# Optimization experiments

Measured on AMD Instinct MI355X. Metric: run time of the kernel, lower is better.

Reference implementation:

```python
import jax, jax.numpy as jnp
import numpy as np

NUM_USERS = 4096
NUM_ITEMS = 4096
NUM_CLASSES = 5
INPUT_DIM = 64
H0 = 64   # hidden[0]
H1 = 32   # hidden[1]
BU = 2048
BV = 2048


def setup_inputs() -> dict:
    key = jax.random.key(0)
    ks = jax.random.split(key, 9)
    ridx = jax.random.randint(ks[0], (NUM_USERS, NUM_ITEMS), 0, NUM_CLASSES * 10)
    ratings = (jnp.arange(NUM_CLASSES)[:, None, None] == ridx[None]).astype(jnp.float32)
    u = jax.random.randint(ks[1], (BU,), 0, NUM_USERS)
    v = jax.random.randint(ks[2], (BV,), 0, NUM_ITEMS)
    u_emb = jax.random.normal(ks[3], (NUM_USERS, INPUT_DIM), jnp.float32) * 0.1
    v_emb = jax.random.normal(ks[4], (NUM_ITEMS, INPUT_DIM), jnp.float32) * 0.1
    gc_w = jax.random.normal(ks[5], (NUM_CLASSES, INPUT_DIM, H0), jnp.float32) / np.sqrt(INPUT_DIM)
    gc_b = jnp.zeros((NUM_CLASSES, H0), jnp.float32)
    dense_w = jax.random.normal(ks[6], (H0, H1), jnp.float32) / np.sqrt(H0)
    dense_b = jnp.zeros((H1,), jnp.float32)
    dec_w = jax.random.normal(ks[7], (NUM_CLASSES, H1, H1), jnp.float32) / np.sqrt(H1)
    return dict(u=u, v=v, ratings=ratings, u_emb=u_emb, v_emb=v_emb,
                gc_w=gc_w, gc_b=gc_b, dense_w=dense_w, dense_b=dense_b, dec_w=dec_w)


def reference(u, v, ratings, u_emb, v_emb, gc_w, gc_b, dense_w, dense_b, dec_w):
    bu = u.shape[0]
    # m = index_select(index_select(ratings, 1, u), 2, v)  -> [C, bu, bv]
    m = ratings[:, u][:, :, v]
    ue = u_emb[u]                      # [bu, D]
    ve = v_emb[v]                      # [bv, D]
    # Degree normalization exactly as in the torch code:
    # du = |sum over dim1 then dim0| -> per-item counts [bv]; di -> per-user counts [bu]
    du = jnp.abs(jnp.sum(m, axis=(0, 1)))
    di = jnp.abs(jnp.sum(m, axis=(0, 2)))
    c = jnp.concatenate([du, di])      # [bv + bu] (requires bu == bv, as in original)
    c = jnp.where(c > 0, 1.0 / c, 0.0)
    x = jnp.concatenate([ue, ve], axis=0)              # [bu+bv, D]
    # Per-class graph convolution, summed over rating classes.
    support = jnp.einsum('nd,cdh->cnh', x, gc_w)       # [C, N, H0]
    su, sv = support[:, :bu], support[:, bu:]
    agg_u = jnp.einsum('cuv,cvh->cuh', m, sv)          # users aggregate items
    agg_v = jnp.einsum('cuv,cuh->cvh', m, su)          # items aggregate users
    agg = jnp.concatenate([agg_u, agg_v], axis=1)      # [C, N, H0]
    z = jnp.sum(c[None, :, None] * agg + gc_b[:, None, :], axis=0)
    z = jax.nn.relu(z)
    hidden = jax.nn.sigmoid(z @ dense_w + dense_b)     # [N, H1]
    hu, hv = hidden[:bu], hidden[bu:]
    # Bilinear decoder: per-class logits u^T W_c v  -> [C, bu, bv]
    logits = jnp.einsum('ud,cde,ve->cuv', hu, dec_w, hv)
    probs = jax.nn.softmax(logits, axis=0)
    classes = jnp.arange(NUM_CLASSES, dtype=hidden.dtype)
    m_hat = jnp.einsum('c,cuv->uv', classes, probs)    # expected rating
    observed = jnp.sum(m, axis=0)                      # [bu, bv] in {0,1}
    n_obs = jnp.maximum(jnp.sum(observed), 1.0)
    logp = jax.nn.log_softmax(logits, axis=0)
    loss = -jnp.sum(m * logp) / n_obs
    pred = jnp.argmax(logits, axis=0)
    true = jnp.argmax(m, axis=0)
    accuracy = jnp.sum((pred == true) * observed) / n_obs
    return m_hat, loss, accuracy
```

## Files before the change

kernel.cpp:

```cpp
#include <hip/hip_runtime.h>
#include <hip/hip_bf16.h>
#include <cstdint>

#define RST 16777216
typedef unsigned short u16;
typedef unsigned char u8;
typedef __attribute__((ext_vector_type(8))) short short8v;
typedef __attribute__((ext_vector_type(4))) float f32x4;

__device__ __forceinline__ u16 f2bf(float x){
  unsigned int b = __float_as_uint(x);
  unsigned int r = (b + 0x7FFFu + ((b >> 16) & 1u)) >> 16;
  return (u16)r;
}
__device__ __forceinline__ float bf2f(u16 h){
  return __uint_as_float(((unsigned int)h) << 16);
}

__global__ __launch_bounds__(256) void k_labels(const int* __restrict__ u, const int* __restrict__ v,
                                                const float* __restrict__ ratings, u8* __restrict__ L,
                                                int* __restrict__ di){
  __shared__ float row[4096];
  __shared__ int wsum[4];
  int i = blockIdx.x;
  int tid = threadIdx.x;
  int lane = tid & 63, wid = tid >> 6;
  int U = u[i];
  int j0 = tid * 8;
  int vj[8];
#pragma unroll
  for (int k = 0; k < 8; k++) vj[k] = v[j0 + k];
  int lab[8];
#pragma unroll
  for (int k = 0; k < 8; k++) lab[k] = 5;
  const float* rbase = ratings + (size_t)U * 4096;
  for (int c = 0; c < 5; c++){
    const float4* src = (const float4*)(rbase + (size_t)c * RST);
#pragma unroll
    for (int k = 0; k < 4; k++) ((float4*)row)[tid + k*256] = src[tid + k*256];
    __syncthreads();
#pragma unroll
    for (int k = 0; k < 8; k++) if (row[vj[k]] > 0.5f) lab[k] = c;
    __syncthreads();
  }
  unsigned int lo = 0, hi = 0;
  int cnt = 0;
#pragma unroll
  for (int k = 0; k < 4; k++){
    lo |= ((unsigned)lab[k]) << (8*k); hi |= ((unsigned)lab[k+4]) << (8*k);
    cnt += (lab[k] != 5); cnt += (lab[k+4] != 5);
  }
  *(uint2*)(L + (size_t)i * 2048 + j0) = make_uint2(lo, hi);
#pragma unroll
  for (int o = 32; o > 0; o >>= 1) cnt += __shfl_down(cnt, o);
  if (lane == 0) wsum[wid] = cnt;
  __syncthreads();
  if (tid == 0) di[i] = wsum[0] + wsum[1] + wsum[2] + wsum[3];
}

__global__ __launch_bounds__(256) void k_trsup(const u8* __restrict__ L, u8* __restrict__ LT,
    const int* __restrict__ u, const int* __restrict__ v,
    const float* __restrict__ u_emb, const float* __restrict__ v_emb, const float* __restrict__ gc_w,
    float* __restrict__ S){
  __shared__ u8 tile[64][64];
  int tid = threadIdx.x;
  if (blockIdx.x < 1024){
    int jb = blockIdx.x & 31, ib = blockIdx.x >> 5;
    int i0 = ib * 64, j0 = jb * 64;
    int r = tid >> 2, cq = tid & 3;
    uint4 d = *(const uint4*)(L + (size_t)(i0 + r) * 2048 + j0 + cq * 16);
    *(uint4*)&tile[r][cq * 16] = d;
    __syncthreads();
    u8 ob[16];
#pragma unroll
    for (int k = 0; k < 16; k++) ob[k] = tile[cq * 16 + k][r];
    *(uint4*)(LT + (size_t)(j0 + r) * 2048 + i0 + cq * 16) = *(uint4*)ob;
  } else {
    int b = blockIdx.x - 1024;
    int c = b >> 6, nblk = b & 63;
    int lane = tid & 63, wid = tid >> 6;
    int n0 = nblk * 64 + wid * 16;
    float w[64];
#pragma unroll
    for (int d = 0; d < 64; d++) w[d] = gc_w[c * 4096 + d * 64 + lane];
    for (int k = 0; k < 16; k++){
      int n = n0 + k;
      int idx = (n < 2048) ? u[n] : v[n - 2048];
      const float* xr = (n < 2048) ? (u_emb + (size_t)idx * 64) : (v_emb + (size_t)idx * 64);
      float xv = xr[lane];
      float acc = 0.f;
#pragma unroll
      for (int d = 0; d < 64; d++) acc += __shfl(xv, d) * w[d];
      S[((size_t)c * 4096 + n) * 64 + lane] = acc;
    }
  }
}

__global__ __launch_bounds__(256) void k_agg(const u8* __restrict__ L, const u8* __restrict__ LT,
    const float* __restrict__ S, float* __restrict__ aggsum, int* __restrict__ du){
  __shared__ u16 lst[2048];
  __shared__ int wbase[4];
  __shared__ float red[4][64];
  int r = blockIdx.x;
  int tid = threadIdx.x;
  int lane = tid & 63, wid = tid >> 6;
  bool uside = (r < 2048);
  const u8* rowp = uside ? (L + (size_t)r * 2048) : (LT + (size_t)(r - 2048) * 2048);
  uint2 d = ((const uint2*)rowp)[tid];
  int lab[8];
#pragma unroll
  for (int k = 0; k < 4; k++){ lab[k] = (d.x >> (8*k)) & 255; lab[k+4] = (d.y >> (8*k)) & 255; }
  int cnt = 0;
#pragma unroll
  for (int k = 0; k < 8; k++) cnt += (lab[k] != 5);
  int pre = cnt;
#pragma unroll
  for (int o = 1; o < 64; o <<= 1){ int t = __shfl_up(pre, o); if (lane >= o) pre += t; }
  if (lane == 63) wbase[wid] = pre;
  __syncthreads();
  int base = 0;
#pragma unroll
  for (int w = 0; w < 4; w++) base += (w < wid) ? wbase[w] : 0;
  int total = wbase[0] + wbase[1] + wbase[2] + wbase[3];
  int off = base + (pre - cnt);
  int j0 = tid * 8;
#pragma unroll
  for (int k = 0; k < 8; k++)
    if (lab[k] != 5) lst[off++] = (u16)(((j0 + k) << 3) | lab[k]);
  if (!uside && tid == 0) du[r - 2048] = total;
  __syncthreads();
  const float* Sop = S + (uside ? 131072 : 0) + lane;
  int e0 = (wid * total) >> 2, e1 = ((wid + 1) * total) >> 2;
  float a0 = 0.f, a1 = 0.f, a2 = 0.f, a3 = 0.f;
  int e = e0;
  for (; e + 4 <= e1; e += 4){
    int x0 = lst[e], x1 = lst[e+1], x2 = lst[e+2], x3 = lst[e+3];
    a0 += Sop[(size_t)(x0 & 7) * 262144 + (size_t)(x0 >> 3) * 64];
    a1 += Sop[(size_t)(x1 & 7) * 262144 + (size_t)(x1 >> 3) * 64];
    a2 += Sop[(size_t)(x2 & 7) * 262144 + (size_t)(x2 >> 3) * 64];
    a3 += Sop[(size_t)(x3 & 7) * 262144 + (size_t)(x3 >> 3) * 64];
  }
  for (; e < e1; e++){
    int x = lst[e];
    a0 += Sop[(size_t)(x & 7) * 262144 + (size_t)(x >> 3) * 64];
  }
  red[wid][lane] = (a0 + a1) + (a2 + a3);
  __syncthreads();
  if (wid == 0) aggsum[(size_t)r * 64 + lane] = red[0][lane] + red[1][lane] + red[2][lane] + red[3][lane];
}

__global__ __launch_bounds__(256) void k_hidden(const float* __restrict__ aggsum, const int* __restrict__ du, const int* __restrict__ di,
    const float* __restrict__ gc_b, const float* __restrict__ dense_w, const float* __restrict__ dense_b,
    float* __restrict__ hidden){
  int wid = threadIdx.x >> 6, lane = threadIdx.x & 63;
  int r = blockIdx.x * 4 + wid;
  float a = aggsum[(size_t)r * 64 + lane];
  int cnt = (r < 2048) ? du[r] : di[r - 2048];
  float inv = (cnt > 0) ? (1.0f / (float)cnt) : 0.0f;
  float bsum = 0.f;
#pragma unroll
  for (int c = 0; c < 5; c++) bsum += gc_b[c * 64 + lane];
  float z = fmaxf(a * inv + bsum, 0.f);
  __shared__ float zb[4][64];
  zb[wid][lane] = z;
  __syncthreads();
  if (lane < 32){
    float s = dense_b[lane];
#pragma unroll
    for (int h = 0; h < 64; h++) s += zb[wid][h] * dense_w[h * 32 + lane];
    hidden[(size_t)r * 32 + lane] = 1.0f / (1.0f + __expf(-s));
  }
}

#define EPI(l, lab, outp) do{ \
  float mx = fmaxf(fmaxf(fmaxf(l[0], l[1]), fmaxf(l[2], l[3])), l[4]); \
  float e0 = __expf(l[0]-mx), e1 = __expf(l[1]-mx), e2 = __expf(l[2]-mx), e3 = __expf(l[3]-mx), e4 = __expf(l[4]-mx); \
  float ssum = e0 + e1 + e2 + e3 + e4; \
  *(outp) = (e1 + 2.f*e2 + 3.f*e3 + 4.f*e4) / ssum; \
  if ((lab) < 5){ \
    int pred = 0; float bm = l[0]; \
    if (l[1] > bm){ bm = l[1]; pred = 1; } \
    if (l[2] > bm){ bm = l[2]; pred = 2; } \
    if (l[3] > bm){ bm = l[3]; pred = 3; } \
    if (l[4] > bm){ bm = l[4]; pred = 4; } \
    float ll = (lab)==0 ? l[0] : ((lab)==1 ? l[1] : ((lab)==2 ? l[2] : ((lab)==3 ? l[3] : l[4]))); \
    lsum += __logf(ssum) + mx - ll; \
    acnt += (pred == (lab)); \
  } \
}while(0)

__global__ __launch_bounds__(256) void k_logits(const float* __restrict__ hidden, const float* __restrict__ dec_w,
    const u8* __restrict__ L, float* __restrict__ mhat, float* __restrict__ lpart, int* __restrict__ apart){
  __shared__ float hu_s[512];
  __shared__ float tsf[5 * 16 * 36];
  int tid = threadIdx.x;
  int lane = tid & 63, w = tid >> 6;
  int i0 = blockIdx.y * 16;
  if (tid < 128) ((float4*)hu_s)[tid] = ((const float4*)(hidden + (size_t)i0 * 32))[tid];
  __syncthreads();
  for (int idx = tid; idx < 2560; idx += 256){
    int c = idx >> 9; int rem = idx & 511; int ii = rem >> 5; int e = rem & 31;
    const float* wc = dec_w + (size_t)c * 1024 + e;
    const float* hr = hu_s + ii * 32;
    float s = 0.f;
#pragma unroll
    for (int d = 0; d < 32; d++) s += hr[d] * wc[d * 32];
    tsf[(c * 16 + ii) * 36 + e] = s;
  }
  __syncthreads();
  int m = lane & 15, q = lane >> 4;
  short8v a_hi[5], a_lo[5];
#pragma unroll
  for (int c = 0; c < 5; c++){
    const float* p = &tsf[(c * 16 + m) * 36 + q * 8];
    float4 f0 = *(const float4*)p;
    float4 f1 = *(const float4*)(p + 4);
    float fa[8] = {f0.x, f0.y, f0.z, f0.w, f1.x, f1.y, f1.z, f1.w};
    short8v hi, lo;
#pragma unroll
    for (int e = 0; e < 8; e++){
      u16 h = f2bf(fa[e]);
      hi[e] = (short)h;
      lo[e] = (short)f2bf(fa[e] - bf2f(h));
    }
    a_hi[c] = hi; a_lo[c] = lo;
  }
  const float* hv = hidden + 2048 * 32;
  float lsum = 0.f; int acnt = 0;
  int jw0 = blockIdx.x * 256 + w * 64;
#pragma unroll
  for (int jj = 0; jj < 4; jj++){
    int j0 = jw0 + jj * 16;
    const float* pb = hv + (size_t)(j0 + m) * 32 + q * 8;
    float4 g0 = *(const float4*)pb;
    float4 g1 = *(const float4*)(pb + 4);
    float fb[8] = {g0.x, g0.y, g0.z, g0.w, g1.x, g1.y, g1.z, g1.w};
    short8v b_hi, b_lo;
#pragma unroll
    for (int e = 0; e < 8; e++){
      u16 h = f2bf(fb[e]);
      b_hi[e] = (short)h;
      b_lo[e] = (short)f2bf(fb[e] - bf2f(h));
    }
    f32x4 acc[5];
    f32x4 z4 = {0.f, 0.f, 0.f, 0.f};
#pragma unroll
    for (int c = 0; c < 5; c++){
      f32x4 a = __builtin_amdgcn_mfma_f32_16x16x32_bf16(a_hi[c], b_hi, z4, 0, 0, 0);
      a = __builtin_amdgcn_mfma_f32_16x16x32_bf16(a_hi[c], b_lo, a, 0, 0, 0);
      a = __builtin_amdgcn_mfma_f32_16x16x32_bf16(a_lo[c], b_hi, a, 0, 0, 0);
      acc[c] = a;
    }
    int jcol = j0 + m;
#pragma unroll
    for (int r = 0; r < 4; r++){
      int irow = i0 + q * 4 + r;
      float l5[5] = {acc[0][r], acc[1][r], acc[2][r], acc[3][r], acc[4][r]};
      int lab = L[(size_t)irow * 2048 + jcol];
      EPI(l5, lab, mhat + (size_t)irow * 2048 + jcol);
    }
  }
#pragma unroll
  for (int o = 32; o > 0; o >>= 1){ lsum += __shfl_down(lsum, o); acnt += __shfl_down(acnt, o); }
  __shared__ float wl[4]; __shared__ int wa[4];
  if (lane == 0){ wl[w] = lsum; wa[w] = acnt; }
  __syncthreads();
  if (tid == 0){
    int pb = blockIdx.y * 8 + blockIdx.x;
    lpart[pb] = wl[0] + wl[1] + wl[2] + wl[3];
    apart[pb] = wa[0] + wa[1] + wa[2] + wa[3];
  }
}

__global__ __launch_bounds__(256) void k_final(const float* __restrict__ lpart, const int* __restrict__ apart,
                                               const int* __restrict__ di, float* __restrict__ out){
  __shared__ float lred[256];
  __shared__ int ared[256], nred[256];
  int tid = threadIdx.x;
  float ls = 0.f; int as = 0;
#pragma unroll
  for (int k = 0; k < 4; k++){ ls += lpart[tid + k * 256]; as += apart[tid + k * 256]; }
  int ns = 0;
#pragma unroll
  for (int k = 0; k < 8; k++) ns += di[tid + k * 256];
  lred[tid] = ls; ared[tid] = as; nred[tid] = ns;
  __syncthreads();
  for (int s = 128; s > 0; s >>= 1){
    if (tid < s){ lred[tid] += lred[tid + s]; ared[tid] += ared[tid + s]; nred[tid] += nred[tid + s]; }
    __syncthreads();
  }
  if (tid == 0){
    float n = fmaxf((float)nred[0], 1.0f);
    out[0] = lred[0] / n;
    out[1] = ((float)ared[0]) / n;
  }
}

extern "C" void kernel_launch(void* const* d_in, const int* in_sizes, int n_in,
                              void* d_out, int out_size, void* d_ws, size_t ws_size,
                              hipStream_t stream){
  const int*   u       = (const int*)d_in[0];
  const int*   v       = (const int*)d_in[1];
  const float* ratings = (const float*)d_in[2];
  const float* u_emb   = (const float*)d_in[3];
  const float* v_emb   = (const float*)d_in[4];
  const float* gc_w    = (const float*)d_in[5];
  const float* gc_b    = (const float*)d_in[6];
  const float* dense_w = (const float*)d_in[7];
  const float* dense_b = (const float*)d_in[8];
  const float* dec_w   = (const float*)d_in[9];
  float* out = (float*)d_out;
  char* ws = (char*)d_ws;

  u8*    L       = (u8*)(ws + 0);
  u8*    LT      = (u8*)(ws + 4194304);
  float* S       = (float*)(ws + 8388608);
  float* aggsum  = (float*)(ws + 13631488);
  float* hidden  = (float*)(ws + 14680064);
  int*   du      = (int*)(ws + 15204352);
  int*   di      = (int*)(ws + 15212544);
  float* lpart   = (float*)(ws + 15220736);
  int*   apart   = (int*)(ws + 15224832);

  k_labels <<<2048, 256, 0, stream>>>(u, v, ratings, L, di);
  k_trsup  <<<1344, 256, 0, stream>>>(L, LT, u, v, u_emb, v_emb, gc_w, S);
  k_agg    <<<4096, 256, 0, stream>>>(L, LT, S, aggsum, du);
  k_hidden <<<1024, 256, 0, stream>>>(aggsum, du, di, gc_b, dense_w, dense_b, hidden);
  k_logits <<<dim3(8, 128), 256, 0, stream>>>(hidden, dec_w, L, out, lpart, apart);
  k_final  <<<1, 256, 0, stream>>>(lpart, apart, di, out + 4194304);
}
```

Before: 114.6 us.

## Fuse aggregation with hidden layer and fold final reduction into logits kernel

Merges the aggregation kernel with the dense/sigmoid hidden kernel, so the per-row aggregate stays in shared memory and is no longer round-tripped through global memory. For user rows, the item-degree count is now recomputed inside the fused kernel by scanning a transposed row. The final loss/accuracy reduction moves into the logits kernel through a last-block-done atomic counter, which removes two launches. In exchange, user-side blocks do an extra row read and reduction, and the kernel relies on threadfence/atomic ordering.

```diff
diff --git a/kernel.cpp b/kernel.cpp
--- a/kernel.cpp
+++ b/kernel.cpp
@@ -61,9 +61,10 @@
 __global__ __launch_bounds__(256) void k_trsup(const u8* __restrict__ L, u8* __restrict__ LT,
     const int* __restrict__ u, const int* __restrict__ v,
     const float* __restrict__ u_emb, const float* __restrict__ v_emb, const float* __restrict__ gc_w,
-    float* __restrict__ S){
+    float* __restrict__ S, int* __restrict__ done_cnt){
   __shared__ u8 tile[64][64];
   int tid = threadIdx.x;
+  if (blockIdx.x == 0 && tid == 0) *done_cnt = 0;
   if (blockIdx.x < 1024){
     int jb = blockIdx.x & 31, ib = blockIdx.x >> 5;
     int i0 = ib * 64, j0 = jb * 64;
@@ -96,15 +97,33 @@
   }
 }
 
-__global__ __launch_bounds__(256) void k_agg(const u8* __restrict__ L, const u8* __restrict__ LT,
-    const float* __restrict__ S, float* __restrict__ aggsum, int* __restrict__ du){
+__global__ __launch_bounds__(256) void k_aggh(const u8* __restrict__ L, const u8* __restrict__ LT,
+    const float* __restrict__ S, const int* __restrict__ di,
+    const float* __restrict__ gc_b, const float* __restrict__ dense_w, const float* __restrict__ dense_b,
+    float* __restrict__ hidden){
   __shared__ u16 lst[2048];
   __shared__ int wbase[4];
   __shared__ float red[4][64];
+  __shared__ float zb[64];
   int r = blockIdx.x;
   int tid = threadIdx.x;
   int lane = tid & 63, wid = tid >> 6;
   bool uside = (r < 2048);
+  int denom;
+  if (uside){
+    uint2 dd = ((const uint2*)(LT + (size_t)r * 2048))[tid];
+    int c2 = 0;
+#pragma unroll
+    for (int k = 0; k < 4; k++){ c2 += (((dd.x >> (8*k)) & 255) != 5); c2 += (((dd.y >> (8*k)) & 255) != 5); }
+#pragma unroll
+    for (int o = 32; o > 0; o >>= 1) c2 += __shfl_down(c2, o);
+    if (lane == 0) wbase[wid] = c2;
+    __syncthreads();
+    denom = wbase[0] + wbase[1] + wbase[2] + wbase[3];
+    __syncthreads();
+  } else {
+    denom = di[r - 2048];
+  }
   const u8* rowp = uside ? (L + (size_t)r * 2048) : (LT + (size_t)(r - 2048) * 2048);
   uint2 d = ((const uint2*)rowp)[tid];
   int lab[8];
@@ -127,7 +146,6 @@
 #pragma unroll
   for (int k = 0; k < 8; k++)
     if (lab[k] != 5) lst[off++] = (u16)(((j0 + k) << 3) | lab[k]);
-  if (!uside && tid == 0) du[r - 2048] = total;
   __syncthreads();
   const float* Sop = S + (uside ? 131072 : 0) + lane;
   int e0 = (wid * total) >> 2, e1 = ((wid + 1) * total) >> 2;
@@ -146,28 +164,19 @@
   }
   red[wid][lane] = (a0 + a1) + (a2 + a3);
   __syncthreads();
-  if (wid == 0) aggsum[(size_t)r * 64 + lane] = red[0][lane] + red[1][lane] + red[2][lane] + red[3][lane];
-}
-
-__global__ __launch_bounds__(256) void k_hidden(const float* __restrict__ aggsum, const int* __restrict__ du, const int* __restrict__ di,
-    const float* __restrict__ gc_b, const float* __restrict__ dense_w, const float* __restrict__ dense_b,
-    float* __restrict__ hidden){
-  int wid = threadIdx.x >> 6, lane = threadIdx.x & 63;
-  int r = blockIdx.x * 4 + wid;
-  float a = aggsum[(size_t)r * 64 + lane];
-  int cnt = (r < 2048) ? du[r] : di[r - 2048];
-  float inv = (cnt > 0) ? (1.0f / (float)cnt) : 0.0f;
   float bsum = 0.f;
 #pragma unroll
   for (int c = 0; c < 5; c++) bsum += gc_b[c * 64 + lane];
-  float z = fmaxf(a * inv + bsum, 0.f);
-  __shared__ float zb[4][64];
-  zb[wid][lane] = z;
-  __syncthreads();
-  if (lane < 32){
+  if (wid == 0){
+    float asum = red[0][lane] + red[1][lane] + red[2][lane] + red[3][lane];
+    float inv = (denom > 0) ? (1.0f / (float)denom) : 0.0f;
+    zb[lane] = fmaxf(asum * inv + bsum, 0.f);
+  }
+  __syncthreads();
+  if (wid == 0 && lane < 32){
     float s = dense_b[lane];
 #pragma unroll
-    for (int h = 0; h < 64; h++) s += zb[wid][h] * dense_w[h * 32 + lane];
+    for (int h = 0; h < 64; h++) s += zb[h] * dense_w[h * 32 + lane];
     hidden[(size_t)r * 32 + lane] = 1.0f / (1.0f + __expf(-s));
   }
 }
@@ -190,7 +199,8 @@
 }while(0)
 
 __global__ __launch_bounds__(256) void k_logits(const float* __restrict__ hidden, const float* __restrict__ dec_w,
-    const u8* __restrict__ L, float* __restrict__ mhat, float* __restrict__ lpart, int* __restrict__ apart){
+    const u8* __restrict__ L, float* __restrict__ mhat, float* __restrict__ lpart, int* __restrict__ apart,
+    int* __restrict__ done_cnt, const int* __restrict__ di, float* __restrict__ out2){
   __shared__ float hu_s[512];
   __shared__ float tsf[5 * 16 * 36];
   int tid = threadIdx.x;
@@ -265,34 +275,35 @@
   __shared__ float wl[4]; __shared__ int wa[4];
   if (lane == 0){ wl[w] = lsum; wa[w] = acnt; }
   __syncthreads();
+  __shared__ int is_last;
   if (tid == 0){
     int pb = blockIdx.y * 8 + blockIdx.x;
     lpart[pb] = wl[0] + wl[1] + wl[2] + wl[3];
     apart[pb] = wa[0] + wa[1] + wa[2] + wa[3];
-  }
-}
-
-__global__ __launch_bounds__(256) void k_final(const float* __restrict__ lpart, const int* __restrict__ apart,
-                                               const int* __restrict__ di, float* __restrict__ out){
-  __shared__ float lred[256];
-  __shared__ int ared[256], nred[256];
-  int tid = threadIdx.x;
-  float ls = 0.f; int as = 0;
-#pragma unroll
-  for (int k = 0; k < 4; k++){ ls += lpart[tid + k * 256]; as += apart[tid + k * 256]; }
-  int ns = 0;
-#pragma unroll
-  for (int k = 0; k < 8; k++) ns += di[tid + k * 256];
-  lred[tid] = ls; ared[tid] = as; nred[tid] = ns;
-  __syncthreads();
-  for (int s = 128; s > 0; s >>= 1){
-    if (tid < s){ lred[tid] += lred[tid + s]; ared[tid] += ared[tid + s]; nred[tid] += nred[tid + s]; }
-    __syncthreads();
-  }
-  if (tid == 0){
-    float n = fmaxf((float)nred[0], 1.0f);
-    out[0] = lred[0] / n;
-    out[1] = ((float)ared[0]) / n;
+    __threadfence();
+    is_last = (atomicAdd(done_cnt, 1) == 1023);
+  }
+  __syncthreads();
+  if (is_last){
+    __threadfence();
+    __shared__ float lred[256];
+    __shared__ int ared[256], nred[256];
+    float ls = 0.f; int as = 0, ns = 0;
+#pragma unroll
+    for (int k = 0; k < 4; k++){ ls += lpart[tid + k * 256]; as += apart[tid + k * 256]; }
+#pragma unroll
+    for (int k = 0; k < 8; k++) ns += di[tid + k * 256];
+    lred[tid] = ls; ared[tid] = as; nred[tid] = ns;
+    __syncthreads();
+    for (int s = 128; s > 0; s >>= 1){
+      if (tid < s){ lred[tid] += lred[tid + s]; ared[tid] += ared[tid + s]; nred[tid] += nred[tid + s]; }
+      __syncthreads();
+    }
+    if (tid == 0){
+      float n = fmaxf((float)nred[0], 1.0f);
+      out2[0] = lred[0] / n;
+      out2[1] = ((float)nred[0] ? ((float)ared[0]) / n : 0.f);
+    }
   }
 }
 
@@ -315,17 +326,14 @@
   u8*    L       = (u8*)(ws + 0);
   u8*    LT      = (u8*)(ws + 4194304);
   float* S       = (float*)(ws + 8388608);
-  float* aggsum  = (float*)(ws + 13631488);
-  float* hidden  = (float*)(ws + 14680064);
-  int*   du      = (int*)(ws + 15204352);
-  int*   di      = (int*)(ws + 15212544);
-  float* lpart   = (float*)(ws + 15220736);
-  int*   apart   = (int*)(ws + 15224832);
+  float* hidden  = (float*)(ws + 13631488);
+  int*   di      = (int*)(ws + 14155776);
+  float* lpart   = (float*)(ws + 14163968);
+  int*   apart   = (int*)(ws + 14168064);
+  int*   done_cnt= (int*)(ws + 14172160);
 
   k_labels <<<2048, 256, 0, stream>>>(u, v, ratings, L, di);
-  k_trsup  <<<1344, 256, 0, stream>>>(L, LT, u, v, u_emb, v_emb, gc_w, S);
-  k_agg    <<<4096, 256, 0, stream>>>(L, LT, S, aggsum, du);
-  k_hidden <<<1024, 256, 0, stream>>>(aggsum, du, di, gc_b, dense_w, dense_b, hidden);
-  k_logits <<<dim3(8, 128), 256, 0, stream>>>(hidden, dec_w, L, out, lpart, apart);
-  k_final  <<<1, 256, 0, stream>>>(lpart, apart, di, out + 4194304);
-}
+  k_trsup  <<<1344, 256, 0, stream>>>(L, LT, u, v, u_emb, v_emb, gc_w, S, done_cnt);
+  k_aggh   <<<4096, 256, 0, stream>>>(L, LT, S, di, gc_b, dense_w, dense_b, hidden);
+  k_logits <<<dim3(8, 128), 256, 0, stream>>>(hidden, dec_w, L, out, lpart, apart, done_cnt, di, out + 4194304);
+}
```

New measurement: 140.6 us. 1.23x slower.
